# Performance work log

Measured on AMD Instinct MI355X. Metric: run time of the kernel, lower is better.

The kernel has to match this reference:

```python
import jax, jax.numpy as jnp
from jax import lax
import numpy as np

N = 10000      # nodes
T = 60         # lookback window
F = 16         # features per timestep
HL = 256       # lstm hidden dim
GH = 8         # gat heads
GC = 64        # gat out channels per head
GD = GH * GC   # 512 concat dim
FH = 512       # fusion hidden
E = 320000     # edges (before self loops)


def _lstm_layer(x, w_ih, w_hh, b_ih, b_hh):
    # x: [T, N, in] -> hidden sequence [T, N, HL]; torch gate order i,f,g,o
    n = x.shape[1]
    h0 = jnp.zeros((n, HL), x.dtype)
    def step(carry, xt):
        h, c = carry
        g = xt @ w_ih.T + h @ w_hh.T + b_ih + b_hh
        i, f, gg, o = jnp.split(g, 4, axis=-1)
        c = jax.nn.sigmoid(f) * c + jax.nn.sigmoid(i) * jnp.tanh(gg)
        h = jax.nn.sigmoid(o) * jnp.tanh(c)
        return (h, c), h
    _, hs = lax.scan(step, (h0, h0), x)
    return hs


def _gatv2(x, src, dst, ea, wl, bl, wr, br, we, att, bias):
    # GATv2Conv (concat=True, edge_dim=1, negative_slope=0.2); self loops already in src/dst/ea
    n = x.shape[0]
    xl = (x @ wl + bl).reshape(n, GH, GC)   # lin_l (source / x_j)
    xr = (x @ wr + br).reshape(n, GH, GC)   # lin_r (target / x_i)
    ee = (ea @ we).reshape(-1, GH, GC)      # lin_edge (bias=False)
    m = jax.nn.leaky_relu(xl[src] + xr[dst] + ee, 0.2)      # [E', GH, GC]
    logits = jnp.einsum('ehc,hc->eh', m, att)               # [E', GH]
    mx = jax.ops.segment_max(logits, dst, num_segments=n)
    ex = jnp.exp(logits - mx[dst])
    den = jax.ops.segment_sum(ex, dst, num_segments=n)
    alpha = ex / den[dst]                                   # softmax over in-edges per node
    out = jax.ops.segment_sum(xl[src] * alpha[..., None], dst, num_segments=n)
    return out.reshape(n, GD) + bias


def setup_inputs():
    key = jax.random.key(0)
    ks = jax.random.split(key, 20)
    f32 = jnp.float32
    def nrm(k, shp, fan):
        return jax.random.normal(k, shp, f32) * (1.0 / np.sqrt(fan))
    return {
        "x_seq": jax.random.normal(ks[0], (N, T, F), f32),
        "edge_index": jax.random.randint(ks[1], (2, E), 0, N, jnp.int32),
        "edge_attr": jax.random.uniform(ks[2], (E, 1), dtype=f32),
        "w_ih0": nrm(ks[3], (4 * HL, F), HL), "w_hh0": nrm(ks[4], (4 * HL, HL), HL),
        "b_ih0": jnp.zeros((4 * HL,), f32), "b_hh0": jnp.zeros((4 * HL,), f32),
        "w_ih1": nrm(ks[5], (4 * HL, HL), HL), "w_hh1": nrm(ks[6], (4 * HL, HL), HL),
        "b_ih1": jnp.zeros((4 * HL,), f32), "b_hh1": jnp.zeros((4 * HL,), f32),
        "g0_wl": nrm(ks[7], (HL, GD), HL), "g0_bl": jnp.zeros((GD,), f32),
        "g0_wr": nrm(ks[8], (HL, GD), HL), "g0_br": jnp.zeros((GD,), f32),
        "g0_we": nrm(ks[9], (1, GD), 1),
        "g0_att": nrm(ks[10], (GH, GC), GC), "g0_bias": jnp.zeros((GD,), f32),
        "g1_wl": nrm(ks[11], (GD, GD), GD), "g1_bl": jnp.zeros((GD,), f32),
        "g1_wr": nrm(ks[12], (GD, GD), GD), "g1_br": jnp.zeros((GD,), f32),
        "g1_we": nrm(ks[13], (1, GD), 1),
        "g1_att": nrm(ks[14], (GH, GC), GC), "g1_bias": jnp.zeros((GD,), f32),
        "fc1_w": nrm(ks[15], (HL + GD, FH), HL + GD), "fc1_b": jnp.zeros((FH,), f32),
        "fc2_w": nrm(ks[16], (FH, 1), FH), "fc2_b": jnp.zeros((1,), f32),
    }


def reference(x_seq, edge_index, edge_attr,
              w_ih0, w_hh0, b_ih0, b_hh0, w_ih1, w_hh1, b_ih1, b_hh1,
              g0_wl, g0_bl, g0_wr, g0_br, g0_we, g0_att, g0_bias,
              g1_wl, g1_bl, g1_wr, g1_br, g1_we, g1_att, g1_bias,
              fc1_w, fc1_b, fc2_w, fc2_b):
    # 2-layer LSTM encoder, take last timestep hidden (dropout off: eval mode)
    xt = jnp.transpose(x_seq, (1, 0, 2))            # [T, N, F]
    h1 = _lstm_layer(xt, w_ih0, w_hh0, b_ih0, b_hh0)
    h2 = _lstm_layer(h1, w_ih1, w_hh1, b_ih1, b_hh1)
    node = h2[-1]                                    # [N, HL]
    # add self loops; fill edge_attr for loops with mean (PyG default fill_value='mean')
    loop = jnp.arange(N, dtype=edge_index.dtype)
    src = jnp.concatenate([edge_index[0], loop])
    dst = jnp.concatenate([edge_index[1], loop])
    ea = jnp.concatenate([edge_attr, jnp.broadcast_to(edge_attr.mean(axis=0), (N, 1))], axis=0)
    g = jax.nn.elu(_gatv2(node, src, dst, ea, g0_wl, g0_bl, g0_wr, g0_br, g0_we, g0_att, g0_bias))
    g = jax.nn.elu(_gatv2(g, src, dst, ea, g1_wl, g1_bl, g1_wr, g1_br, g1_we, g1_att, g1_bias))
    fused = jnp.concatenate([node, g], axis=1)       # [N, HL+GD]
    h = jax.nn.relu(fused @ fc1_w + fc1_b)
    return h @ fc2_w + fc2_b                         # [N, 1]
```

## Files before the change

### kernel.cpp

```cpp
#include <hip/hip_runtime.h>

#define DEV __device__ __forceinline__

typedef _Float16 f16;
typedef _Float16 f16x8 __attribute__((ext_vector_type(8)));
typedef _Float16 f16x2 __attribute__((ext_vector_type(2)));
typedef float f32x4 __attribute__((ext_vector_type(4)));

DEV float sigmoidf_(float x) { return 1.0f / (1.0f + __expf(-x)); }
DEV float tanhf2_(float x)   { return 1.0f - 2.0f / (__expf(2.0f * x) + 1.0f); }

DEV void load_lds16(const void* g, void* l) {
    __builtin_amdgcn_global_load_lds(
        (const __attribute__((address_space(1))) char*)(const char*)g,
        (__attribute__((address_space(3))) char*)(unsigned int)(unsigned long long)(char*)l,
        16, 0, 0);
}

DEV int swz(int row, int ck) { return ck ^ (row & 3) ^ ((row >> 2) & 3); }

__global__ void prep_w0_kernel(const float* __restrict__ wih,
                               const float* __restrict__ whh,
                               f16* __restrict__ dst) {
    int idx = blockIdx.x * 256 + threadIdx.x;
    if (idx >= 1024 * 288) return;
    int rd = idx / 288, k = idx - rd * 288;
    int T = rd >> 7, p = rd & 127;
    int u = T * 32 + ((p >> 6) & 1) * 16 + (p & 15);
    int g = (p >> 4) & 3;
    int src = g * 256 + u;
    float v;
    if (k < 16)        v = wih[src * 16 + k];
    else if (k < 272)  v = whh[src * 256 + (k - 16)];
    else               v = 0.f;
    dst[idx] = (f16)v;
}

__global__ void prep_w1_kernel(const float* __restrict__ wih,
                               const float* __restrict__ whh,
                               f16* __restrict__ dst) {
    int idx = blockIdx.x * 256 + threadIdx.x;
    if (idx >= 1024 * 512) return;
    int rd = idx >> 9, k = idx & 511;
    int T = rd >> 7, p = rd & 127;
    int u = T * 32 + ((p >> 6) & 1) * 16 + (p & 15);
    int g = (p >> 4) & 3;
    int src = g * 256 + u;
    float v = (k < 256) ? wih[src * 256 + k] : whh[src * 256 + (k - 256)];
    dst[idx] = (f16)v;
}

__global__ void prep_bias4_kernel(const float* __restrict__ bi,
                                  const float* __restrict__ bh,
                                  float* __restrict__ dst) {
    int idx = blockIdx.x * 256 + threadIdx.x;
    if (idx >= 1024) return;
    int u = idx >> 2, g = idx & 3;
    dst[idx] = bi[g * 256 + u] + bh[g * 256 + u];
}

__global__ void prep_wt_kernel(const float* __restrict__ src, f16* __restrict__ dst,
                               int K, int N) {
    int idx = blockIdx.x * 256 + threadIdx.x;
    if (idx >= K * N) return;
    int n = idx / K, k = idx - n * K;
    dst[idx] = (f16)src[(size_t)k * N + n];
}

__global__ void prep_x0_kernel(const float* __restrict__ x_seq, f16* __restrict__ A0,
                               int Nn) {
    int idx = blockIdx.x * 256 + threadIdx.x;
    if (idx >= Nn * 16) return;
    int m = idx >> 4, f = idx & 15;
    A0[(size_t)m * 288 + f] = (f16)x_seq[(size_t)m * 960 + f];
}

DEV void tile_load_chunk(const f16* __restrict__ A, int lda,
                         const f16* __restrict__ Bt, int K,
                         int m0, int n0, int k0,
                         f16* __restrict__ sA, f16* __restrict__ sB,
                         int w, int arow, int achk)
{
#pragma unroll
    for (int c = 0; c < 2; ++c) {
        int R = c * 64 + w * 16;
        load_lds16(A + (size_t)(m0 + R + arow) * lda + k0 + achk, sA + R * 32);
        load_lds16(Bt + (size_t)(n0 + R + arow) * K + k0 + achk, sB + R * 32);
    }
}

DEV void tile_compute_chunk(const f16* __restrict__ sA, const f16* __restrict__ sB,
                            f32x4 (&acc)[4][4], int wr, int wc, int frow, int fsl)
{
    f16x8 af[4], bf[4];
#pragma unroll
    for (int i = 0; i < 4; ++i)
        af[i] = *(const f16x8*)&sA[(wr + i * 16 + frow) * 32 + fsl];
#pragma unroll
    for (int j = 0; j < 4; ++j)
        bf[j] = *(const f16x8*)&sB[(wc + j * 16 + frow) * 32 + fsl];
#pragma unroll
    for (int i = 0; i < 4; ++i)
#pragma unroll
        for (int j = 0; j < 4; ++j)
            acc[i][j] = __builtin_amdgcn_mfma_f32_16x16x32_f16(af[i], bf[j], acc[i][j], 0, 0, 0);
}

DEV void lstm_step_core(
    f16* __restrict__ sA, f16* __restrict__ sB,
    int bx, int by,
    const f16* __restrict__ A, int lda, int K,
    const f16* __restrict__ Wt,
    const float* __restrict__ bias4,
    float* __restrict__ c_state,
    f16* __restrict__ hA, int ldhA, int offhA,
    f16* __restrict__ hB, int ldhB, int offhB,
    const float* __restrict__ xsrc, int tnext,
    int M)
{
    const int tid = threadIdx.x;
    const int w = tid >> 6, lane = tid & 63;
    const int m0 = bx * 128, n0 = by * 128;
    const int arow = lane >> 2;
    const int achk = swz(arow, lane & 3) * 8;
    const int frow = lane & 15, l4 = lane >> 4;
    const int fsl = swz(frow, l4) * 8;
    const int wr = (w >> 1) * 64, wc = (w & 1) * 64;

    const int u = by * 32 + (w & 1) * 16 + (lane & 15);
    const int rbase = m0 + wr + (lane >> 4) * 4;
    float cold[4][4];
#pragma unroll
    for (int i = 0; i < 4; ++i)
#pragma unroll
        for (int r = 0; r < 4; ++r)
            cold[i][r] = c_state[(size_t)(rbase + i * 16 + r) * 256 + u];

    f32x4 acc[4][4] = {};
    const int nch = K >> 5;

    tile_load_chunk(A, lda, Wt, K, m0, n0, 0, sA, sB, w, arow, achk);
    for (int kc = 0; kc < nch; ++kc) {
        __syncthreads();
        const int cur = (kc & 1) * 4096;
        if (kc + 1 < nch) {
            const int nxt = ((kc + 1) & 1) * 4096;
            tile_load_chunk(A, lda, Wt, K, m0, n0, (kc + 1) * 32,
                            sA + nxt, sB + nxt, w, arow, achk);
        }
        tile_compute_chunk(sA + cur, sB + cur, acc, wr, wc, frow, fsl);
    }

    const float4 bb = *(const float4*)&bias4[u * 4];
#pragma unroll
    for (int i = 0; i < 4; ++i) {
#pragma unroll
        for (int r = 0; r < 4; ++r) {
            int m = rbase + i * 16 + r;
            if (m < M) {
                float gi = sigmoidf_(acc[i][0][r] + bb.x);
                float gf = sigmoidf_(acc[i][1][r] + bb.y);
                float gg = tanhf2_(acc[i][2][r] + bb.z);
                float go = sigmoidf_(acc[i][3][r] + bb.w);
                float cn = gf * cold[i][r] + gi * gg;
                c_state[(size_t)m * 256 + u] = cn;
                f16 h = (f16)(go * tanhf2_(cn));
                hA[(size_t)m * ldhA + offhA + u] = h;
                if (hB) hB[(size_t)m * ldhB + offhB + u] = h;
            }
        }
    }
    if (xsrc && by == 0) {
        int row = tid >> 1, fb = (tid & 1) * 8;
        int m = m0 + row;
        if (m < M) {
            const float* xp = xsrc + (size_t)m * 960 + tnext * 16 + fb;
            f16* dp = hB + (size_t)m * ldhB + fb;
#pragma unroll
            for (int q = 0; q < 8; ++q) dp[q] = (f16)xp[q];
        }
    }
}

__global__ __launch_bounds__(256) void lstm_mfma_kernel(
    const f16* __restrict__ A, int lda, int K,
    const f16* __restrict__ Wt, const float* __restrict__ bias4,
    float* __restrict__ c_state,
    f16* __restrict__ hA, int ldhA, int offhA,
    f16* __restrict__ hB, int ldhB, int offhB,
    const float* __restrict__ xsrc, int tnext, int M, int mtiles)
{
    __shared__ __align__(16) f16 sA[2 * 4096];
    __shared__ __align__(16) f16 sB[2 * 4096];
    const int l = blockIdx.x;
    const int xcd = l & 7, q = l >> 3;
    const int y = q & 7, xhi = q >> 3;
    const int x = xhi * 8 + xcd;
    if (x >= mtiles) return;
    lstm_step_core(sA, sB, x, y, A, lda, K, Wt, bias4, c_state,
                   hA, ldhA, offhA, hB, ldhB, offhB, xsrc, tnext, M);
}

__global__ __launch_bounds__(256) void lstm_dual_kernel(
    const f16* __restrict__ A1, const f16* __restrict__ W1t,
    const float* __restrict__ b41, float* __restrict__ c1,
    f16* __restrict__ h1A, int ldh1A, int offh1A,
    const f16* __restrict__ A0, const f16* __restrict__ W0t,
    const float* __restrict__ b40, float* __restrict__ c0,
    f16* __restrict__ h0A, int ldh0A, int offh0A,
    f16* __restrict__ h0B, int ldh0B, int offh0B,
    const float* __restrict__ xsrc, int tnext, int M, int mtiles)
{
    __shared__ __align__(16) f16 sA[2 * 4096];
    __shared__ __align__(16) f16 sB[2 * 4096];
    const int l = blockIdx.x;
    const int xcd = l & 7, q = l >> 3;
    const int yz = q & 15, xhi = q >> 4;
    const int x = xhi * 8 + xcd;
    if (x >= mtiles) return;
    const int y = yz & 7, z = yz >> 3;
    if (z == 0)
        lstm_step_core(sA, sB, x, y, A1, 512, 512, W1t, b41, c1,
                       h1A, ldh1A, offh1A, nullptr, 0, 0, nullptr, 0, M);
    else
        lstm_step_core(sA, sB, x, y, A0, 288, 288, W0t, b40, c0,
                       h0A, ldh0A, offh0A, h0B, ldh0B, offh0B, xsrc, tnext, M);
}

__global__ __launch_bounds__(256) void gemm16_kernel(
    const f16* __restrict__ A, int lda,
    const f16* __restrict__ Bt, int K,
    const float* __restrict__ bias,
    f16* __restrict__ C16, float* __restrict__ C32, int ldc,
    int act, int M)
{
    __shared__ __align__(16) f16 sA[2 * 4096];
    __shared__ __align__(16) f16 sB[2 * 4096];
    const int tid = threadIdx.x;
    const int w = tid >> 6, lane = tid & 63;
    const int m0 = blockIdx.x * 128, n0 = blockIdx.y * 128;
    const int arow = lane >> 2;
    const int achk = swz(arow, lane & 3) * 8;
    const int frow = lane & 15, l4 = lane >> 4;
    const int fsl = swz(frow, l4) * 8;
    const int wr = (w >> 1) * 64, wcn = (w & 1) * 64;

    f32x4 acc[4][4] = {};
    const int nch = K >> 5;

    tile_load_chunk(A, lda, Bt, K, m0, n0, 0, sA, sB, w, arow, achk);
    for (int kc = 0; kc < nch; ++kc) {
        __syncthreads();
        const int cur = (kc & 1) * 4096;
        if (kc + 1 < nch) {
            const int nxt = ((kc + 1) & 1) * 4096;
            tile_load_chunk(A, lda, Bt, K, m0, n0, (kc + 1) * 32,
                            sA + nxt, sB + nxt, w, arow, achk);
        }
        tile_compute_chunk(sA + cur, sB + cur, acc, wr, wcn, frow, fsl);
    }

    const int rbase = m0 + wr + (lane >> 4) * 4;
#pragma unroll
    for (int i = 0; i < 4; ++i) {
#pragma unroll
        for (int r = 0; r < 4; ++r) {
            int m = rbase + i * 16 + r;
            if (m >= M) continue;
#pragma unroll
            for (int j = 0; j < 4; ++j) {
                int n = n0 + wcn + j * 16 + (lane & 15);
                float v = acc[i][j][r] + bias[n];
                if (act == 1) v = fmaxf(v, 0.f);
                if (C16) C16[(size_t)m * ldc + n] = (f16)v;
                else     C32[(size_t)m * ldc + n] = v;
            }
        }
    }
}

__global__ __launch_bounds__(256) void gemm16_dual_kernel(
    const f16* __restrict__ A, int lda,
    const f16* __restrict__ Btl, const f16* __restrict__ Btr, int K,
    const float* __restrict__ biasl, const float* __restrict__ biasr,
    f16* __restrict__ Cl, f16* __restrict__ Cr, int ldc, int M)
{
    __shared__ __align__(16) f16 sA[2 * 4096];
    __shared__ __align__(16) f16 sB[2 * 4096];
    const int side = blockIdx.y >> 2;
    const f16* Bt = side ? Btr : Btl;
    const float* bias = side ? biasr : biasl;
    f16* C16 = side ? Cr : Cl;
    const int tid = threadIdx.x;
    const int w = tid >> 6, lane = tid & 63;
    const int m0 = blockIdx.x * 128, n0 = (blockIdx.y & 3) * 128;
    const int arow = lane >> 2;
    const int achk = swz(arow, lane & 3) * 8;
    const int frow = lane & 15, l4 = lane >> 4;
    const int fsl = swz(frow, l4) * 8;
    const int wr = (w >> 1) * 64, wcn = (w & 1) * 64;

    f32x4 acc[4][4] = {};
    const int nch = K >> 5;

    tile_load_chunk(A, lda, Bt, K, m0, n0, 0, sA, sB, w, arow, achk);
    for (int kc = 0; kc < nch; ++kc) {
        __syncthreads();
        const int cur = (kc & 1) * 4096;
        if (kc + 1 < nch) {
            const int nxt = ((kc + 1) & 1) * 4096;
            tile_load_chunk(A, lda, Bt, K, m0, n0, (kc + 1) * 32,
                            sA + nxt, sB + nxt, w, arow, achk);
        }
        tile_compute_chunk(sA + cur, sB + cur, acc, wr, wcn, frow, fsl);
    }

    const int rbase = m0 + wr + (lane >> 4) * 4;
#pragma unroll
    for (int i = 0; i < 4; ++i) {
#pragma unroll
        for (int r = 0; r < 4; ++r) {
            int m = rbase + i * 16 + r;
            if (m >= M) continue;
#pragma unroll
            for (int j = 0; j < 4; ++j) {
                int n = n0 + wcn + j * 16 + (lane & 15);
                float v = acc[i][j][r] + bias[n];
                C16[(size_t)m * ldc + n] = (f16)v;
            }
        }
    }
}

__global__ void mean_sum_kernel(const float* __restrict__ a, int n, float* __restrict__ out) {
    __shared__ float s[256];
    float loc = 0.f;
    for (int i = blockIdx.x * 256 + threadIdx.x; i < n; i += gridDim.x * 256) loc += a[i];
    s[threadIdx.x] = loc;
    __syncthreads();
    for (int off = 128; off; off >>= 1) {
        if (threadIdx.x < off) s[threadIdx.x] += s[threadIdx.x + off];
        __syncthreads();
    }
    if (threadIdx.x == 0) atomicAdd(out, s[0]);
}

__global__ void hist_kernel(const int* __restrict__ ei, int Ne, int Nn,
                            int* __restrict__ counts) {
    int e = blockIdx.x * 256 + threadIdx.x;
    if (e >= Ne + Nn) return;
    int d = (e < Ne) ? ei[Ne + e] : (e - Ne);
    atomicAdd(&counts[d], 1);
}

__global__ void scan_kernel(const int* __restrict__ counts, int* __restrict__ offsets, int n) {
    __shared__ int s[256];
    int tid = threadIdx.x;
    int chunk = (n + 255) / 256;
    int b = tid * chunk;
    int loc = 0;
    for (int j = 0; j < chunk; ++j) { int i = b + j; if (i < n) loc += counts[i]; }
    s[tid] = loc;
    __syncthreads();
    for (int off = 1; off < 256; off <<= 1) {
        int v = (tid >= off) ? s[tid - off] : 0;
        __syncthreads();
        s[tid] += v;
        __syncthreads();
    }
    int run = (tid == 0) ? 0 : s[tid - 1];
    for (int j = 0; j < chunk; ++j) {
        int i = b + j;
        if (i < n) { offsets[i] = run; run += counts[i]; }
    }
    if (tid == 255) offsets[n] = run;
}

__global__ void scatter_kernel(const int* __restrict__ ei, const float* __restrict__ ea,
                               const float* __restrict__ sump, float inv_ne, int Ne, int Nn,
                               int* __restrict__ cursor, int* __restrict__ src_sorted,
                               float* __restrict__ ea_sorted) {
    int e = blockIdx.x * 256 + threadIdx.x;
    if (e >= Ne + Nn) return;
    int s, d; float a;
    if (e < Ne) { s = ei[e]; d = ei[Ne + e]; a = ea[e]; }
    else        { s = e - Ne; d = s; a = sump[0] * inv_ne; }
    int pos = atomicAdd(&cursor[d], 1);
    src_sorted[pos] = s;
    ea_sorted[pos] = a;
}

__global__ __launch_bounds__(256) void gat_fused_kernel(
    const f16* __restrict__ xl, const f16* __restrict__ xr,
    const float* __restrict__ we, const float* __restrict__ att,
    const float* __restrict__ bias,
    const int* __restrict__ offsets, const int* __restrict__ src_sorted,
    const float* __restrict__ ea_sorted,
    f16* __restrict__ out, int ldo, int N)
{
    __shared__ float s_acc[8][4][64];
    __shared__ float s_m[4][64];
    __shared__ float s_den[4][64];
    const int i = blockIdx.x;
    const int tid = threadIdx.x;
    const int w = tid >> 6, lane = tid & 63;
    const int c8 = lane * 8;

    f16x8 xrv = *(const f16x8*)&xr[(size_t)i * 512 + c8];
    float xr_[8], we_[8], at_[8];
#pragma unroll
    for (int k = 0; k < 8; ++k) xr_[k] = (float)xrv[k];
    *(float4*)&we_[0] = *(const float4*)&we[c8];
    *(float4*)&we_[4] = *(const float4*)&we[c8 + 4];
    *(float4*)&at_[0] = *(const float4*)&att[c8];
    *(float4*)&at_[4] = *(const float4*)&att[c8 + 4];

    const int beg = offsets[i], end = offsets[i + 1];

    float m = -1e30f, den = 0.f;
    float acc[8] = {};

    int e = beg + w;
    float a = 0.f; f16x8 xv = {};
    if (e < end) {
        a = ea_sorted[e];
        xv = *(const f16x8*)&xl[(size_t)src_sorted[e] * 512 + c8];
    }
    for (; e < end; e += 4) {
        float an = a; f16x8 xvn = xv;
        if (e + 4 < end) {
            int sn = src_sorted[e + 4];
            an = ea_sorted[e + 4];
            xvn = *(const f16x8*)&xl[(size_t)sn * 512 + c8];
        }
        float x[8];
        float p = 0.f;
#pragma unroll
        for (int k = 0; k < 8; ++k) {
            x[k] = (float)xv[k];
            float v = x[k] + xr_[k] + a * we_[k];
            v = (v > 0.f) ? v : 0.2f * v;
            p = fmaf(v, at_[k], p);
        }
        p += __shfl_xor(p, 1);
        p += __shfl_xor(p, 2);
        p += __shfl_xor(p, 4);
        if (__all(p <= m + 8.f)) {
            float wg = __expf(p - m);
            den += wg;
#pragma unroll
            for (int k = 0; k < 8; ++k) acc[k] = fmaf(wg, x[k], acc[k]);
        } else {
            float mn = fmaxf(m, p);
            float r  = __expf(m - mn);
            float wg = __expf(p - mn);
            den = den * r + wg;
#pragma unroll
            for (int k = 0; k < 8; ++k) acc[k] = fmaf(acc[k], r, wg * x[k]);
            m = mn;
        }
        a = an; xv = xvn;
    }

    s_m[w][lane] = m;
    s_den[w][lane] = den;
#pragma unroll
    for (int k = 0; k < 8; ++k) s_acc[k][w][lane] = acc[k];
    __syncthreads();

    const int c2 = tid * 2;
    const int l = c2 >> 3;
    const int k0 = c2 & 7;
    float m0 = s_m[0][l], m1 = s_m[1][l], m2 = s_m[2][l], m3 = s_m[3][l];
    float M = fmaxf(fmaxf(m0, m1), fmaxf(m2, m3));
    float e0 = __expf(m0 - M), e1 = __expf(m1 - M);
    float e2 = __expf(m2 - M), e3 = __expf(m3 - M);
    float D = s_den[0][l] * e0 + s_den[1][l] * e1 + s_den[2][l] * e2 + s_den[3][l] * e3;
    float A0 = s_acc[k0][0][l] * e0 + s_acc[k0][1][l] * e1
             + s_acc[k0][2][l] * e2 + s_acc[k0][3][l] * e3;
    float A1 = s_acc[k0 + 1][0][l] * e0 + s_acc[k0 + 1][1][l] * e1
             + s_acc[k0 + 1][2][l] * e2 + s_acc[k0 + 1][3][l] * e3;
    float rD = 1.f / D;
    float v0 = A0 * rD + bias[c2];
    float v1 = A1 * rD + bias[c2 + 1];
    v0 = (v0 > 0.f) ? v0 : __expf(v0) - 1.f;
    v1 = (v1 > 0.f) ? v1 : __expf(v1) - 1.f;
    f16x2 ov; ov.x = (f16)v0; ov.y = (f16)v1;
    *(f16x2*)&out[(size_t)i * ldo + c2] = ov;
}

__global__ void fc2_kernel(const float* __restrict__ H, const float* __restrict__ w,
                           const float* __restrict__ b, float* __restrict__ out, int N) {
    int wv = threadIdx.x >> 6, lane = threadIdx.x & 63;
    int node = blockIdx.x * 4 + wv;
    if (node >= N) return;
    float s = 0.f;
#pragma unroll
    for (int j = 0; j < 8; ++j)
        s += H[(size_t)node * 512 + j * 64 + lane] * w[j * 64 + lane];
#pragma unroll
    for (int off = 32; off; off >>= 1) s += __shfl_xor(s, off, 64);
    if (lane == 0) out[node] = s + b[0];
}

extern "C" void kernel_launch(void* const* d_in, const int* in_sizes, int n_in,
                              void* d_out, int out_size, void* d_ws, size_t ws_size,
                              hipStream_t stream) {
    const float* x_seq     = (const float*)d_in[0];
    const int*   edge_index= (const int*)d_in[1];
    const float* edge_attr = (const float*)d_in[2];
    const float* w_ih0 = (const float*)d_in[3];
    const float* w_hh0 = (const float*)d_in[4];
    const float* b_ih0 = (const float*)d_in[5];
    const float* b_hh0 = (const float*)d_in[6];
    const float* w_ih1 = (const float*)d_in[7];
    const float* w_hh1 = (const float*)d_in[8];
    const float* b_ih1 = (const float*)d_in[9];
    const float* b_hh1 = (const float*)d_in[10];
    const float* g0_wl = (const float*)d_in[11];
    const float* g0_bl = (const float*)d_in[12];
    const float* g0_wr = (const float*)d_in[13];
    const float* g0_br = (const float*)d_in[14];
    const float* g0_we = (const float*)d_in[15];
    const float* g0_att= (const float*)d_in[16];
    const float* g0_bias=(const float*)d_in[17];
    const float* g1_wl = (const float*)d_in[18];
    const float* g1_bl = (const float*)d_in[19];
    const float* g1_wr = (const float*)d_in[20];
    const float* g1_br = (const float*)d_in[21];
    const float* g1_we = (const float*)d_in[22];
    const float* g1_att= (const float*)d_in[23];
    const float* g1_bias=(const float*)d_in[24];
    const float* fc1_w = (const float*)d_in[25];
    const float* fc1_b = (const float*)d_in[26];
    const float* fc2_w = (const float*)d_in[27];
    const float* fc2_b = (const float*)d_in[28];
    float* out = (float*)d_out;

    const int Nn = in_sizes[0] / (60 * 16);
    const int Ne = in_sizes[1] / 2;
    const int Etot = Ne + Nn;
    const int MT = (Nn + 127) / 128;
    const int Mpad = MT * 128;
    const int MTpad8 = ((MT + 7) / 8) * 8;

    size_t off = 0;
    auto alloc = [&](size_t bytes) -> void* {
        void* r = (char*)d_ws + off;
        off += (bytes + 255) & ~(size_t)255;
        return r;
    };
    f16* W0t   = (f16*)alloc((size_t)1024 * 288 * 2);
    f16* W1t   = (f16*)alloc((size_t)1024 * 512 * 2);
    float* b40 = (float*)alloc(1024 * 4);
    float* b41 = (float*)alloc(1024 * 4);
    f16* Wg0l  = (f16*)alloc((size_t)512 * 256 * 2);
    f16* Wg0r  = (f16*)alloc((size_t)512 * 256 * 2);
    f16* Wg1l  = (f16*)alloc((size_t)512 * 512 * 2);
    f16* Wg1r  = (f16*)alloc((size_t)512 * 512 * 2);
    f16* Wfc1  = (f16*)alloc((size_t)512 * 768 * 2);
    f16* A0b[2]; A0b[0] = (f16*)alloc((size_t)Mpad * 288 * 2);
                 A0b[1] = (f16*)alloc((size_t)Mpad * 288 * 2);
    f16* A1b[2]; A1b[0] = (f16*)alloc((size_t)Mpad * 512 * 2);
                 A1b[1] = (f16*)alloc((size_t)Mpad * 512 * 2);
    float* c0  = (float*)alloc((size_t)Mpad * 256 * 4);
    float* c1  = (float*)alloc((size_t)Mpad * 256 * 4);
    f16* fused = (f16*)alloc((size_t)Mpad * 768 * 2);
    f16* xlbuf = (f16*)alloc((size_t)Mpad * 512 * 2);
    f16* xrbuf = (f16*)alloc((size_t)Mpad * 512 * 2);
    f16* gbuf  = (f16*)alloc((size_t)Mpad * 512 * 2);
    float* hfc1= (float*)alloc((size_t)Mpad * 512 * 4);
    int* counts  = (int*)alloc((size_t)Nn * 4);
    int* offsets = (int*)alloc((size_t)(Nn + 1) * 4);
    int* cursor  = (int*)alloc((size_t)Nn * 4);
    int* src_sorted = (int*)alloc((size_t)Etot * 4);
    float* ea_sorted = (float*)alloc((size_t)Etot * 4);
    float* meanp = (float*)alloc(256);

    prep_w0_kernel<<<dim3((1024 * 288 + 255) / 256), 256, 0, stream>>>(w_ih0, w_hh0, W0t);
    prep_w1_kernel<<<dim3((1024 * 512 + 255) / 256), 256, 0, stream>>>(w_ih1, w_hh1, W1t);
    prep_bias4_kernel<<<dim3(4), 256, 0, stream>>>(b_ih0, b_hh0, b40);
    prep_bias4_kernel<<<dim3(4), 256, 0, stream>>>(b_ih1, b_hh1, b41);
    prep_wt_kernel<<<dim3((256 * 512 + 255) / 256), 256, 0, stream>>>(g0_wl, Wg0l, 256, 512);
    prep_wt_kernel<<<dim3((256 * 512 + 255) / 256), 256, 0, stream>>>(g0_wr, Wg0r, 256, 512);
    prep_wt_kernel<<<dim3((512 * 512 + 255) / 256), 256, 0, stream>>>(g1_wl, Wg1l, 512, 512);
    prep_wt_kernel<<<dim3((512 * 512 + 255) / 256), 256, 0, stream>>>(g1_wr, Wg1r, 512, 512);
    prep_wt_kernel<<<dim3((768 * 512 + 255) / 256), 256, 0, stream>>>(fc1_w, Wfc1, 768, 512);
    hipMemsetAsync(A0b[0], 0, (size_t)Mpad * 288 * 2, stream);
    hipMemsetAsync(A0b[1], 0, (size_t)Mpad * 288 * 2, stream);
    hipMemsetAsync(A1b[0], 0, (size_t)Mpad * 512 * 2, stream);
    hipMemsetAsync(c0, 0, (size_t)Mpad * 256 * 4, stream);
    hipMemsetAsync(c1, 0, (size_t)Mpad * 256 * 4, stream);
    prep_x0_kernel<<<dim3((Nn * 16 + 255) / 256), 256, 0, stream>>>(x_seq, A0b[0], Nn);

    hipMemsetAsync(meanp, 0, 4, stream);
    hipMemsetAsync(counts, 0, (size_t)Nn * 4, stream);
    mean_sum_kernel<<<dim3(256), 256, 0, stream>>>(edge_attr, Ne, meanp);
    hist_kernel<<<dim3((Etot + 255) / 256), 256, 0, stream>>>(edge_index, Ne, Nn, counts);
    scan_kernel<<<dim3(1), 256, 0, stream>>>(counts, offsets, Nn);
    hipMemcpyAsync(cursor, offsets, (size_t)Nn * 4, hipMemcpyDeviceToDevice, stream);
    scatter_kernel<<<dim3((Etot + 255) / 256), 256, 0, stream>>>(
        edge_index, edge_attr, meanp, 1.0f / (float)Ne, Ne, Nn, cursor, src_sorted, ea_sorted);

    const int solo_grid = MTpad8 * 8;
    const int dual_grid = MTpad8 * 16;
    lstm_mfma_kernel<<<dim3(solo_grid), 256, 0, stream>>>(
        A0b[0], 288, 288, W0t, b40, c0,
        A1b[0], 512, 0,
        A0b[1], 288, 16,
        x_seq, 1, Nn, MT);
    for (int k = 0; k < 59; ++k) {
        lstm_dual_kernel<<<dim3(dual_grid), 256, 0, stream>>>(
            A1b[k & 1], W1t, b41, c1,
            A1b[(k + 1) & 1], 512, 256,
            A0b[(k + 1) & 1], W0t, b40, c0,
            A1b[(k + 1) & 1], 512, 0,
            A0b[k & 1], 288, 16,
            (k + 1 < 59) ? x_seq : nullptr, k + 2, Nn, MT);
    }
    lstm_mfma_kernel<<<dim3(solo_grid), 256, 0, stream>>>(
        A1b[1], 512, 512, W1t, b41, c1,
        fused, 768, 0,
        nullptr, 0, 0,
        nullptr, 0, Nn, MT);

    gemm16_dual_kernel<<<dim3(MT, 8), 256, 0, stream>>>(
        fused, 768, Wg0l, Wg0r, 256, g0_bl, g0_br, xlbuf, xrbuf, 512, Nn);
    gat_fused_kernel<<<dim3(Nn), 256, 0, stream>>>(
        xlbuf, xrbuf, g0_we, g0_att, g0_bias, offsets, src_sorted, ea_sorted,
        gbuf, 512, Nn);

    gemm16_dual_kernel<<<dim3(MT, 8), 256, 0, stream>>>(
        gbuf, 512, Wg1l, Wg1r, 512, g1_bl, g1_br, xlbuf, xrbuf, 512, Nn);
    gat_fused_kernel<<<dim3(Nn), 256, 0, stream>>>(
        xlbuf, xrbuf, g1_we, g1_att, g1_bias, offsets, src_sorted, ea_sorted,
        fused + 256, 768, Nn);

    gemm16_kernel<<<dim3(MT, 4), 256, 0, stream>>>(
        fused, 768, Wfc1, 768, fc1_b, nullptr, hfc1, 512, 1, Nn);
    fc2_kernel<<<dim3((Nn + 3) / 4), 256, 0, stream>>>(hfc1, fc2_w, fc2_b, out, Nn);
}
```

Before: 2.822 ms.

## Load GEMM MFMA fragments directly from global memory, deepen GAT gather prefetch

Replaces the LDS double-buffered tile staging (global_load_lds plus swizzle and a barrier per K-chunk) in all MFMA GEMMs, including the LSTM step kernels, with per-wave fragment loads straight from global memory into registers. Loads are software-pipelined two K-chunks deep. This removes shared memory use and __syncthreads, which may raise occupancy. The cost is that the two waves sharing each A or B row now fetch it separately, raising global and L2 traffic. Separately, the GAT aggregation loop now prefetches edges two iterations ahead instead of one to hide gather latency.

```diff
diff --git a/kernel.cpp b/kernel.cpp
--- a/kernel.cpp
+++ b/kernel.cpp
@@ -9,15 +9,6 @@
 
 DEV float sigmoidf_(float x) { return 1.0f / (1.0f + __expf(-x)); }
 DEV float tanhf2_(float x)   { return 1.0f - 2.0f / (__expf(2.0f * x) + 1.0f); }
-
-DEV void load_lds16(const void* g, void* l) {
-    __builtin_amdgcn_global_load_lds(
-        (const __attribute__((address_space(1))) char*)(const char*)g,
-        (__attribute__((address_space(3))) char*)(unsigned int)(unsigned long long)(char*)l,
-        16, 0, 0);
-}
-
-DEV int swz(int row, int ck) { return ck ^ (row & 3) ^ ((row >> 2) & 3); }
 
 __global__ void prep_w0_kernel(const float* __restrict__ wih,
                                const float* __restrict__ whh,
@@ -75,39 +66,51 @@
     A0[(size_t)m * 288 + f] = (f16)x_seq[(size_t)m * 960 + f];
 }
 
-DEV void tile_load_chunk(const f16* __restrict__ A, int lda,
-                         const f16* __restrict__ Bt, int K,
-                         int m0, int n0, int k0,
-                         f16* __restrict__ sA, f16* __restrict__ sB,
-                         int w, int arow, int achk)
-{
-#pragma unroll
-    for (int c = 0; c < 2; ++c) {
-        int R = c * 64 + w * 16;
-        load_lds16(A + (size_t)(m0 + R + arow) * lda + k0 + achk, sA + R * 32);
-        load_lds16(Bt + (size_t)(n0 + R + arow) * K + k0 + achk, sB + R * 32);
-    }
-}
-
-DEV void tile_compute_chunk(const f16* __restrict__ sA, const f16* __restrict__ sB,
-                            f32x4 (&acc)[4][4], int wr, int wc, int frow, int fsl)
-{
-    f16x8 af[4], bf[4];
+DEV void frag_load(const f16* __restrict__ p, int stride, f16x8 (&f)[4]) {
+    f[0] = *(const f16x8*)(p);
+    f[1] = *(const f16x8*)(p + (size_t)stride * 16);
+    f[2] = *(const f16x8*)(p + (size_t)stride * 32);
+    f[3] = *(const f16x8*)(p + (size_t)stride * 48);
+}
+
+DEV void frag_mfma(const f16x8 (&a)[4], const f16x8 (&b)[4], f32x4 (&acc)[4][4]) {
 #pragma unroll
     for (int i = 0; i < 4; ++i)
-        af[i] = *(const f16x8*)&sA[(wr + i * 16 + frow) * 32 + fsl];
-#pragma unroll
-    for (int j = 0; j < 4; ++j)
-        bf[j] = *(const f16x8*)&sB[(wc + j * 16 + frow) * 32 + fsl];
-#pragma unroll
-    for (int i = 0; i < 4; ++i)
 #pragma unroll
         for (int j = 0; j < 4; ++j)
-            acc[i][j] = __builtin_amdgcn_mfma_f32_16x16x32_f16(af[i], bf[j], acc[i][j], 0, 0, 0);
+            acc[i][j] = __builtin_amdgcn_mfma_f32_16x16x32_f16(a[i], b[j], acc[i][j], 0, 0, 0);
+}
+
+DEV void gemm_reg(const f16* __restrict__ A, int lda,
+                  const f16* __restrict__ Bt, int K,
+                  int m0, int n0, f32x4 (&acc)[4][4])
+{
+    const int tid = threadIdx.x;
+    const int w = tid >> 6, lane = tid & 63;
+    const int frow = lane & 15, l4 = lane >> 4;
+    const int wr = (w >> 1) * 64, wc = (w & 1) * 64;
+    const f16* ap = A + (size_t)(m0 + wr + frow) * lda + l4 * 8;
+    const f16* bp = Bt + (size_t)(n0 + wc + frow) * K + l4 * 8;
+    const int nch = K >> 5;
+
+    f16x8 aA[4], bA[4], aB[4], bB[4];
+    frag_load(ap, lda, aA);
+    frag_load(bp, K, bA);
+    int kc = 0;
+    for (; kc + 2 <= nch; kc += 2) {
+        frag_load(ap + (kc + 1) * 32, lda, aB);
+        frag_load(bp + (kc + 1) * 32, K, bB);
+        frag_mfma(aA, bA, acc);
+        if (kc + 2 < nch) {
+            frag_load(ap + (kc + 2) * 32, lda, aA);
+            frag_load(bp + (kc + 2) * 32, K, bA);
+        }
+        frag_mfma(aB, bB, acc);
+    }
+    if (kc < nch) frag_mfma(aA, bA, acc);
 }
 
 DEV void lstm_step_core(
-    f16* __restrict__ sA, f16* __restrict__ sB,
     int bx, int by,
     const f16* __restrict__ A, int lda, int K,
     const f16* __restrict__ Wt,
@@ -121,11 +124,7 @@
     const int tid = threadIdx.x;
     const int w = tid >> 6, lane = tid & 63;
     const int m0 = bx * 128, n0 = by * 128;
-    const int arow = lane >> 2;
-    const int achk = swz(arow, lane & 3) * 8;
-    const int frow = lane & 15, l4 = lane >> 4;
-    const int fsl = swz(frow, l4) * 8;
-    const int wr = (w >> 1) * 64, wc = (w & 1) * 64;
+    const int wr = (w >> 1) * 64;
 
     const int u = by * 32 + (w & 1) * 16 + (lane & 15);
     const int rbase = m0 + wr + (lane >> 4) * 4;
@@ -137,19 +136,7 @@
             cold[i][r] = c_state[(size_t)(rbase + i * 16 + r) * 256 + u];
 
     f32x4 acc[4][4] = {};
-    const int nch = K >> 5;
-
-    tile_load_chunk(A, lda, Wt, K, m0, n0, 0, sA, sB, w, arow, achk);
-    for (int kc = 0; kc < nch; ++kc) {
-        __syncthreads();
-        const int cur = (kc & 1) * 4096;
-        if (kc + 1 < nch) {
-            const int nxt = ((kc + 1) & 1) * 4096;
-            tile_load_chunk(A, lda, Wt, K, m0, n0, (kc + 1) * 32,
-                            sA + nxt, sB + nxt, w, arow, achk);
-        }
-        tile_compute_chunk(sA + cur, sB + cur, acc, wr, wc, frow, fsl);
-    }
+    gemm_reg(A, lda, Wt, K, m0, n0, acc);
 
     const float4 bb = *(const float4*)&bias4[u * 4];
 #pragma unroll
@@ -190,14 +177,12 @@
     f16* __restrict__ hB, int ldhB, int offhB,
     const float* __restrict__ xsrc, int tnext, int M, int mtiles)
 {
-    __shared__ __align__(16) f16 sA[2 * 4096];
-    __shared__ __align__(16) f16 sB[2 * 4096];
     const int l = blockIdx.x;
     const int xcd = l & 7, q = l >> 3;
     const int y = q & 7, xhi = q >> 3;
     const int x = xhi * 8 + xcd;
     if (x >= mtiles) return;
-    lstm_step_core(sA, sB, x, y, A, lda, K, Wt, bias4, c_state,
+    lstm_step_core(x, y, A, lda, K, Wt, bias4, c_state,
                    hA, ldhA, offhA, hB, ldhB, offhB, xsrc, tnext, M);
 }
 
@@ -211,8 +196,6 @@
     f16* __restrict__ h0B, int ldh0B, int offh0B,
     const float* __restrict__ xsrc, int tnext, int M, int mtiles)
 {
-    __shared__ __align__(16) f16 sA[2 * 4096];
-    __shared__ __align__(16) f16 sB[2 * 4096];
     const int l = blockIdx.x;
     const int xcd = l & 7, q = l >> 3;
     const int yz = q & 15, xhi = q >> 4;
@@ -220,10 +203,10 @@
     if (x >= mtiles) return;
     const int y = yz & 7, z = yz >> 3;
     if (z == 0)
-        lstm_step_core(sA, sB, x, y, A1, 512, 512, W1t, b41, c1,
+        lstm_step_core(x, y, A1, 512, 512, W1t, b41, c1,
                        h1A, ldh1A, offh1A, nullptr, 0, 0, nullptr, 0, M);
     else
-        lstm_step_core(sA, sB, x, y, A0, 288, 288, W0t, b40, c0,
+        lstm_step_core(x, y, A0, 288, 288, W0t, b40, c0,
                        h0A, ldh0A, offh0A, h0B, ldh0B, offh0B, xsrc, tnext, M);
 }
 
@@ -234,31 +217,13 @@
     f16* __restrict__ C16, float* __restrict__ C32, int ldc,
     int act, int M)
 {
-    __shared__ __align__(16) f16 sA[2 * 4096];
-    __shared__ __align__(16) f16 sB[2 * 4096];
     const int tid = threadIdx.x;
     const int w = tid >> 6, lane = tid & 63;
     const int m0 = blockIdx.x * 128, n0 = blockIdx.y * 128;
-    const int arow = lane >> 2;
-    const int achk = swz(arow, lane & 3) * 8;
-    const int frow = lane & 15, l4 = lane >> 4;
-    const int fsl = swz(frow, l4) * 8;
     const int wr = (w >> 1) * 64, wcn = (w & 1) * 64;
 
     f32x4 acc[4][4] = {};
-    const int nch = K >> 5;
-
-    tile_load_chunk(A, lda, Bt, K, m0, n0, 0, sA, sB, w, arow, achk);
-    for (int kc = 0; kc < nch; ++kc) {
-        __syncthreads();
-        const int cur = (kc & 1) * 4096;
-        if (kc + 1 < nch) {
-            const int nxt = ((kc + 1) & 1) * 4096;
-            tile_load_chunk(A, lda, Bt, K, m0, n0, (kc + 1) * 32,
-                            sA + nxt, sB + nxt, w, arow, achk);
-        }
-        tile_compute_chunk(sA + cur, sB + cur, acc, wr, wcn, frow, fsl);
-    }
+    gemm_reg(A, lda, Bt, K, m0, n0, acc);
 
     const int rbase = m0 + wr + (lane >> 4) * 4;
 #pragma unroll
@@ -285,8 +250,6 @@
     const float* __restrict__ biasl, const float* __restrict__ biasr,
     f16* __restrict__ Cl, f16* __restrict__ Cr, int ldc, int M)
 {
-    __shared__ __align__(16) f16 sA[2 * 4096];
-    __shared__ __align__(16) f16 sB[2 * 4096];
     const int side = blockIdx.y >> 2;
     const f16* Bt = side ? Btr : Btl;
     const float* bias = side ? biasr : biasl;
@@ -294,26 +257,10 @@
     const int tid = threadIdx.x;
     const int w = tid >> 6, lane = tid & 63;
     const int m0 = blockIdx.x * 128, n0 = (blockIdx.y & 3) * 128;
-    const int arow = lane >> 2;
-    const int achk = swz(arow, lane & 3) * 8;
-    const int frow = lane & 15, l4 = lane >> 4;
-    const int fsl = swz(frow, l4) * 8;
     const int wr = (w >> 1) * 64, wcn = (w & 1) * 64;
 
     f32x4 acc[4][4] = {};
-    const int nch = K >> 5;
-
-    tile_load_chunk(A, lda, Bt, K, m0, n0, 0, sA, sB, w, arow, achk);
-    for (int kc = 0; kc < nch; ++kc) {
-        __syncthreads();
-        const int cur = (kc & 1) * 4096;
-        if (kc + 1 < nch) {
-            const int nxt = ((kc + 1) & 1) * 4096;
-            tile_load_chunk(A, lda, Bt, K, m0, n0, (kc + 1) * 32,
-                            sA + nxt, sB + nxt, w, arow, achk);
-        }
-        tile_compute_chunk(sA + cur, sB + cur, acc, wr, wcn, frow, fsl);
-    }
+    gemm_reg(A, lda, Bt, K, m0, n0, acc);
 
     const int rbase = m0 + wr + (lane >> 4) * 4;
 #pragma unroll
@@ -421,17 +368,23 @@
     float acc[8] = {};
 
     int e = beg + w;
-    float a = 0.f; f16x8 xv = {};
+    float a_c = 0.f, a_n = 0.f;
+    f16x8 xv_c = {}, xv_n = {};
     if (e < end) {
-        a = ea_sorted[e];
-        xv = *(const f16x8*)&xl[(size_t)src_sorted[e] * 512 + c8];
+        a_c = ea_sorted[e];
+        xv_c = *(const f16x8*)&xl[(size_t)src_sorted[e] * 512 + c8];
+    }
+    if (e + 4 < end) {
+        a_n = ea_sorted[e + 4];
+        xv_n = *(const f16x8*)&xl[(size_t)src_sorted[e + 4] * 512 + c8];
     }
     for (; e < end; e += 4) {
-        float an = a; f16x8 xvn = xv;
-        if (e + 4 < end) {
-            int sn = src_sorted[e + 4];
-            an = ea_sorted[e + 4];
-            xvn = *(const f16x8*)&xl[(size_t)sn * 512 + c8];
+        float a = a_c; f16x8 xv = xv_c;
+        a_c = a_n; xv_c = xv_n;
+        if (e + 8 < end) {
+            int sn = src_sorted[e + 8];
+            a_n = ea_sorted[e + 8];
+            xv_n = *(const f16x8*)&xl[(size_t)sn * 512 + c8];
         }
         float x[8];
         float p = 0.f;
@@ -459,7 +412,6 @@
             for (int k = 0; k < 8; ++k) acc[k] = fmaf(acc[k], r, wg * x[k]);
             m = mn;
         }
-        a = an; xv = xvn;
     }
 
     s_m[w][lane] = m;
```

New measurement: 4.758 ms. +68.6%, slower.
